# Optimization experiments

Measured on AMD Instinct MI355X. Metric: run time of the kernel, lower is better.

Reference implementation:

```python
import jax, jax.numpy as jnp
import numpy as np

B, T, IN, H = 4096, 19, 17, 1024


def setup_inputs() -> dict:
    key = jax.random.key(0)
    ks = jax.random.split(key, 7)
    s = 0.05
    return {
        "x": jax.random.normal(ks[0], (B, T, IN), dtype=jnp.float32),
        "W_ih": jax.random.normal(ks[1], (4 * H, IN), dtype=jnp.float32) * s,
        "W_hh": jax.random.normal(ks[2], (4 * H, H), dtype=jnp.float32) * s,
        "b_ih": jax.random.normal(ks[3], (4 * H,), dtype=jnp.float32) * s,
        "b_hh": jax.random.normal(ks[4], (4 * H,), dtype=jnp.float32) * s,
        "W_lin": jax.random.normal(ks[5], (IN, H), dtype=jnp.float32) * s,
        "b_lin": jax.random.normal(ks[6], (IN,), dtype=jnp.float32) * s,
    }


def reference(x, W_ih, W_hh, b_ih, b_hh, W_lin, b_lin):
    # x: [B, T, IN]; PyTorch LSTMCell gate order is i, f, g, o.
    batch = x.shape[0]
    hid = W_hh.shape[1]
    h0 = jnp.zeros((batch, hid), dtype=x.dtype)
    c0 = jnp.zeros((batch, hid), dtype=x.dtype)

    def step(carry, xt):
        h, c = carry
        gates = xt @ W_ih.T + b_ih + h @ W_hh.T + b_hh  # [B, 4H]
        i, f, g, o = jnp.split(gates, 4, axis=-1)
        i = jax.nn.sigmoid(i)
        f = jax.nn.sigmoid(f)
        g = jnp.tanh(g)
        o = jax.nn.sigmoid(o)
        c_new = f * c + i * g
        h_new = o * jnp.tanh(c_new)
        out = h_new @ W_lin.T + b_lin  # [B, IN]
        return (h_new, c_new), out

    (h_fin, c_fin), outs = jax.lax.scan(step, (h0, c0), jnp.swapaxes(x, 0, 1))
    output = jnp.swapaxes(outs, 0, 1)  # [B, T, IN]
    return output, h_fin, c_fin
```

## Files before the change

kernel.cpp:

```cpp
#include <hip/hip_runtime.h>
#include <hip/hip_bf16.h>

typedef unsigned short u16;
typedef __attribute__((ext_vector_type(8))) __bf16 bf16x8;
typedef __attribute__((ext_vector_type(8))) short short8;
typedef __attribute__((ext_vector_type(4))) float f32x4;

#define BB 4096
#define TT 19
#define INP 17
#define HH 1024
#define NE 4128
#define NT_PROJ 15

#define ABASE(b) ((b) * 16384)
#define BBASE(b) (32768 + (b) * 16384)
#define PBASE(b) (65536 + (b) * 2048)
#define LDS_BYTES 139264

#define FENCE asm volatile("" ::: "memory")

__device__ __forceinline__ u16 f2bfu(float f) {
    __hip_bfloat16 b = __float2bfloat16(f);
    return __builtin_bit_cast(unsigned short, b);
}
__device__ __forceinline__ float fast_sigmoid(float x) {
    return 1.f / (1.f + __expf(-x));
}
__device__ __forceinline__ float fast_tanh(float x) {
    float e = __expf(2.f * x);
    return (e - 1.f) / (e + 1.f);
}
__device__ __forceinline__ bf16x8 ldfrag(const u16* p) {
    return __builtin_bit_cast(bf16x8, *(const short8*)p);
}
__device__ __forceinline__ void cp16(const u16* l, const void* g) {
    __builtin_amdgcn_global_load_lds(
        (const __attribute__((address_space(1))) unsigned int*)g,
        (__attribute__((address_space(3))) unsigned int*)l, 16, 0, 0);
}

__global__ void prep_wperm(const float* __restrict__ Whh, const float* __restrict__ Wlin,
                           u16* __restrict__ wperm) {
    size_t idx = ((size_t)blockIdx.x * 256 + threadIdx.x) * 8;
    int R = (int)(idx >> 10);
    int k = (int)(idx & 1023);
    const float* src = nullptr;
    if (R < 4096) {
        int nt = R >> 8, r = R & 255;
        int qn = r >> 6, nf = (r >> 4) & 3, cj = r & 15;
        int hcol = nt * 64 + qn * 16 + cj;
        src = Whh + ((size_t)(nf * HH + hcol)) * HH + k;
    } else if (R - 4096 < INP) {
        src = Wlin + (size_t)(R - 4096) * HH + k;
    }
#pragma unroll
    for (int e = 0; e < 8; ++e) wperm[idx + e] = src ? f2bfu(src[e]) : (u16)0;
}

__global__ void prep_wx64(const float* __restrict__ Wih, u16* __restrict__ wx64) {
    int idx = blockIdx.x * 256 + threadIdx.x;
    int R = idx >> 6, k = idx & 63;
    u16 v = 0;
    if (R < 4096 && k < INP) {
        int nt = R >> 8, r = R & 255;
        int qn = r >> 6, nf = (r >> 4) & 3, cj = r & 15;
        int hcol = nt * 64 + qn * 16 + cj;
        v = f2bfu(Wih[(size_t)(nf * HH + hcol) * INP + k]);
    }
    wx64[idx] = v;
}

__global__ void prep_bias(const float* __restrict__ bih, const float* __restrict__ bhh,
                          float* __restrict__ bias) {
    int idx = blockIdx.x * 256 + threadIdx.x;
    bias[idx] = bih[idx] + bhh[idx];
}

__global__ void prep_x64(const float* __restrict__ x, u16* __restrict__ xpad) {
    int idx = blockIdx.x * 256 + threadIdx.x;
    int c = idx & 63;
    int rb = idx >> 6;
    int t = rb >> 12;
    int b = rb & 4095;
    xpad[idx] = (c < INP) ? f2bfu(x[((size_t)b * TT + t) * INP + c]) : (u16)0;
}

__global__ __launch_bounds__(512, 2) void lstm_step(
    const u16* __restrict__ h_in, u16* __restrict__ h_out,
    float* __restrict__ c_buf, const u16* __restrict__ wperm,
    const u16* __restrict__ wx64, const float* __restrict__ bias,
    const u16* __restrict__ xpad64, const float* __restrict__ blin,
    float* __restrict__ outp, float* __restrict__ h_fin,
    int t, int is_last, int tail)
{
    extern __shared__ u16 lds[];

    const int tid = threadIdx.x;
    const int lane = tid & 63;
    const int wv = tid >> 6;
    const int qr = wv >> 2, qn = wv & 3;
    const int r16 = lane & 15, s4 = lane >> 4;

    int mt, nt;
    if (tail) { mt = blockIdx.x; nt = NT_PROJ; }
    else {
        const int xcd = blockIdx.x & 7, local = blockIdx.x >> 3;
        mt = (xcd >> 2) * 8 + (local & 7);
        nt = (xcd & 3) * 4 + (local >> 3);
    }
    const int m0 = mt * 256;
    const size_t R0 = (size_t)nt * 256;
    const bool my_proj = (nt == NT_PROJ) && (qn < 2);

    int srow[4], sgc[4];
#pragma unroll
    for (int i = 0; i < 4; ++i) {
        int d = tid + i * 512;
        srow[i] = d >> 3;
        sgc[i] = (d & 7) ^ (srow[i] & 7);
    }
    const u16* hA[4];
    const u16* wB[4];
#pragma unroll
    for (int i = 0; i < 4; ++i) {
        hA[i] = h_in + (size_t)(m0 + srow[i]) * HH + sgc[i] * 8;
        wB[i] = wperm + (R0 + srow[i]) * HH + sgc[i] * 8;
    }
    const int prow = (tid >> 3) & 31;
    const int pgc = (tid & 7) ^ (prow & 7);
    const u16* wP = wperm + (size_t)(4096 + prow) * HH + pgc * 8;

    int aoff[8], boff[4], poff;
#pragma unroll
    for (int mf = 0; mf < 8; ++mf) {
        int r = qr * 128 + mf * 16 + r16;
        aoff[mf] = r * 64 + ((s4 ^ (r & 7)) * 8);
    }
#pragma unroll
    for (int nf = 0; nf < 4; ++nf) {
        int r = qn * 64 + nf * 16 + r16;
        boff[nf] = r * 64 + ((s4 ^ (r & 7)) * 8);
    }
    {
        int r = qn * 16 + r16;
        poff = r * 64 + ((s4 ^ (r & 7)) * 8);
    }

    f32x4 acc[8][4];
    const int n = nt * 64 + qn * 16 + r16;
    if (!tail) {
#pragma unroll
        for (int nf = 0; nf < 4; ++nf) {
            float bv = bias[nf * HH + n];
#pragma unroll
            for (int mf = 0; mf < 8; ++mf) acc[mf][nf] = (f32x4){bv, bv, bv, bv};
        }
    }
    f32x4 pacc[8];
    const int p = qn * 16 + r16;
    if (my_proj) {
        float pv = (p < INP) ? blin[p] : 0.f;
#pragma unroll
        for (int mf = 0; mf < 8; ++mf) pacc[mf] = (f32x4){pv, pv, pv, pv};
    }

    const u16* xA = xpad64 + ((size_t)t * BB + m0) * 64;
#pragma unroll
    for (int i = 0; i < 4; ++i)
        cp16(&lds[ABASE(0) + (tid + i * 512) * 8], xA + (size_t)srow[i] * 64 + sgc[i] * 8);
#pragma unroll
    for (int i = 0; i < 4; ++i)
        cp16(&lds[BBASE(0) + (tid + i * 512) * 8], wx64 + (R0 + srow[i]) * 64 + sgc[i] * 8);
    if (wv < 4) cp16(&lds[PBASE(0) + tid * 8], wP);

    for (int j = 0; j < 17; ++j) {
        const int cb = j & 1, nb = cb ^ 1;
        if (j < 16) {
            const int ko = j * 64;
#pragma unroll
            for (int i = 0; i < 4; ++i)
                cp16(&lds[ABASE(nb) + (tid + i * 512) * 8], hA[i] + ko);
#pragma unroll
            for (int i = 0; i < 4; ++i)
                cp16(&lds[BBASE(nb) + (tid + i * 512) * 8], wB[i] + ko);
            if (wv < 4) {
                cp16(&lds[PBASE(nb) + tid * 8], wP + ko);
                asm volatile("s_waitcnt vmcnt(9)" ::: "memory");
            } else {
                asm volatile("s_waitcnt vmcnt(8)" ::: "memory");
            }
        } else {
            asm volatile("s_waitcnt vmcnt(0)" ::: "memory");
        }
        __builtin_amdgcn_s_barrier();
        FENCE;

        const int cbA = ABASE(cb), cbB = BBASE(cb), cbP = PBASE(cb);
        const bool do_p = my_proj && (j > 0);
#pragma unroll
        for (int kk = 0; kk < 2; ++kk) {
            const int kx = kk * 32;
            bf16x8 b[4];
            if (!tail) {
#pragma unroll
                for (int nf = 0; nf < 4; ++nf)
                    b[nf] = ldfrag(&lds[cbB + (boff[nf] ^ kx)]);
            }
            bf16x8 pb;
            if (do_p) pb = ldfrag(&lds[cbP + (poff ^ kx)]);
#pragma unroll
            for (int h2 = 0; h2 < 2; ++h2) {
                bf16x8 a[4];
#pragma unroll
                for (int i = 0; i < 4; ++i)
                    a[i] = ldfrag(&lds[cbA + (aoff[h2 * 4 + i] ^ kx)]);
                if (!tail) {
#pragma unroll
                    for (int nf = 0; nf < 4; ++nf)
#pragma unroll
                        for (int i = 0; i < 4; ++i)
                            acc[h2 * 4 + i][nf] = __builtin_amdgcn_mfma_f32_16x16x32_bf16(
                                a[i], b[nf], acc[h2 * 4 + i][nf], 0, 0, 0);
                }
                if (do_p) {
#pragma unroll
                    for (int i = 0; i < 4; ++i)
                        pacc[h2 * 4 + i] = __builtin_amdgcn_mfma_f32_16x16x32_bf16(
                            a[i], pb, pacc[h2 * 4 + i], 0, 0, 0);
                }
            }
        }
        FENCE;
        __builtin_amdgcn_s_barrier();
        FENCE;
    }

    if (!tail) {
#pragma unroll
        for (int mf = 0; mf < 8; ++mf)
#pragma unroll
            for (int j = 0; j < 4; ++j) {
                int row = m0 + qr * 128 + mf * 16 + s4 * 4 + j;
                float iv = fast_sigmoid(acc[mf][0][j]);
                float fv = fast_sigmoid(acc[mf][1][j]);
                float gv = fast_tanh(acc[mf][2][j]);
                float ov = fast_sigmoid(acc[mf][3][j]);
                size_t ci = (size_t)row * HH + n;
                float cold = __builtin_nontemporal_load(&c_buf[ci]);
                float cnew = fv * cold + iv * gv;
                float hnew = ov * fast_tanh(cnew);
                __builtin_nontemporal_store(cnew, &c_buf[ci]);
                h_out[ci] = f2bfu(hnew);
                if (is_last) __builtin_nontemporal_store(hnew, &h_fin[ci]);
            }
    }
    if (my_proj && t > 0 && p < INP) {
#pragma unroll
        for (int mf = 0; mf < 8; ++mf)
#pragma unroll
            for (int j = 0; j < 4; ++j) {
                int row = m0 + qr * 128 + mf * 16 + s4 * 4 + j;
                __builtin_nontemporal_store(
                    pacc[mf][j], &outp[((size_t)row * TT + (t - 1)) * INP + p]);
            }
    }
}

extern "C" void kernel_launch(void* const* d_in, const int* in_sizes, int n_in,
                              void* d_out, int out_size, void* d_ws, size_t ws_size,
                              hipStream_t stream)
{
    const float* x    = (const float*)d_in[0];
    const float* Wih  = (const float*)d_in[1];
    const float* Whh  = (const float*)d_in[2];
    const float* bih  = (const float*)d_in[3];
    const float* bhh  = (const float*)d_in[4];
    const float* Wlin = (const float*)d_in[5];
    const float* blin = (const float*)d_in[6];
    float* out = (float*)d_out;

    char* ws = (char*)d_ws;
    u16* hb0     = (u16*)(ws);
    u16* hb1     = (u16*)(ws +  8388608);
    u16* xpad64  = (u16*)(ws + 16777216);
    u16* wperm   = (u16*)(ws + 27262976);
    u16* wx64    = (u16*)(ws + 35717120);
    float* bias  = (float*)(ws + 36245504);

    float* h_fin = out + (size_t)BB * TT * INP;
    float* c_buf = h_fin + (size_t)BB * HH;

    hipFuncSetAttribute((const void*)lstm_step,
                        hipFuncAttributeMaxDynamicSharedMemorySize, LDS_BYTES);

    hipMemsetAsync(hb0, 0, (size_t)BB * HH * sizeof(u16), stream);
    hipMemsetAsync(c_buf, 0, (size_t)BB * HH * sizeof(float), stream);
    hipMemsetAsync((char*)xpad64 + (size_t)19 * BB * 64 * 2, 0, BB * 64 * 2, stream);

    prep_wperm<<<2064, 256, 0, stream>>>(Whh, Wlin, wperm);
    prep_wx64<<<1032, 256, 0, stream>>>(Wih, wx64);
    prep_bias<<<16, 256, 0, stream>>>(bih, bhh, bias);
    prep_x64<<<19456, 256, 0, stream>>>(x, xpad64);

    for (int t = 0; t < TT; ++t) {
        const u16* hin = (t & 1) ? hb1 : hb0;
        u16* hout = (t & 1) ? hb0 : hb1;
        lstm_step<<<256, 512, LDS_BYTES, stream>>>(
            hin, hout, c_buf, wperm, wx64, bias, xpad64, blin, out,
            h_fin, t, (t == TT - 1) ? 1 : 0, 0);
    }
    lstm_step<<<16, 512, LDS_BYTES, stream>>>(
        hb1, hb0, c_buf, wperm, wx64, bias, xpad64, blin, out,
        h_fin, TT, 0, 1);
}
```

Measured before the change: 1.165 ms.

## Prefetch cell state into LDS and coalesce c/h epilogue stores

```diff
diff --git a/kernel.cpp b/kernel.cpp
--- a/kernel.cpp
+++ b/kernel.cpp
@@ -33,6 +33,9 @@
 }
 __device__ __forceinline__ bf16x8 ldfrag(const u16* p) {
     return __builtin_bit_cast(bf16x8, *(const short8*)p);
+}
+__device__ __forceinline__ int cBase(int row) {
+    return row < 128 ? 16384 + row * 128 : 49152 + (row - 128) * 128;
 }
 __device__ __forceinline__ void cp16(const u16* l, const void* g) {
     __builtin_amdgcn_global_load_lds(
@@ -190,6 +193,15 @@
             } else {
                 asm volatile("s_waitcnt vmcnt(8)" ::: "memory");
             }
+        } else if (!tail) {
+#pragma unroll
+            for (int i = 0; i < 8; ++i) {
+                const int s = tid + i * 512;
+                const int crow = s >> 4, cch = s & 15;
+                const u16* dst = (i < 4) ? &lds[16384 + s * 8] : &lds[32768 + s * 8];
+                cp16(dst, c_buf + (size_t)(m0 + crow) * HH + nt * 64 + cch * 4);
+            }
+            asm volatile("s_waitcnt vmcnt(8)" ::: "memory");
         } else {
             asm volatile("s_waitcnt vmcnt(0)" ::: "memory");
         }
@@ -198,6 +210,7 @@
 
         const int cbA = ABASE(cb), cbB = BBASE(cb), cbP = PBASE(cb);
         const bool do_p = my_proj && (j > 0);
+        __builtin_amdgcn_s_setprio(1);
 #pragma unroll
         for (int kk = 0; kk < 2; ++kk) {
             const int kx = kk * 32;
@@ -231,29 +244,43 @@
                 }
             }
         }
+        __builtin_amdgcn_s_setprio(0);
         FENCE;
         __builtin_amdgcn_s_barrier();
         FENCE;
     }
 
     if (!tail) {
+        asm volatile("s_waitcnt vmcnt(0)" ::: "memory");
+        __syncthreads();
+        const int cl = qn * 16 + r16;
 #pragma unroll
         for (int mf = 0; mf < 8; ++mf)
 #pragma unroll
             for (int j = 0; j < 4; ++j) {
-                int row = m0 + qr * 128 + mf * 16 + s4 * 4 + j;
+                int rl = qr * 128 + mf * 16 + s4 * 4 + j;
                 float iv = fast_sigmoid(acc[mf][0][j]);
                 float fv = fast_sigmoid(acc[mf][1][j]);
                 float gv = fast_tanh(acc[mf][2][j]);
                 float ov = fast_sigmoid(acc[mf][3][j]);
-                size_t ci = (size_t)row * HH + n;
-                float cold = __builtin_nontemporal_load(&c_buf[ci]);
+                float* crow = (float*)&lds[cBase(rl)];
+                float cold = crow[cl];
                 float cnew = fv * cold + iv * gv;
                 float hnew = ov * fast_tanh(cnew);
-                __builtin_nontemporal_store(cnew, &c_buf[ci]);
-                h_out[ci] = f2bfu(hnew);
-                if (is_last) __builtin_nontemporal_store(hnew, &h_fin[ci]);
-            }
+                crow[cl] = cnew;
+                lds[rl * 64 + cl] = f2bfu(hnew);
+                if (is_last)
+                    __builtin_nontemporal_store(
+                        hnew, &h_fin[(size_t)(m0 + rl) * HH + n]);
+            }
+        __syncthreads();
+#pragma unroll 4
+        for (int r = 0; r < 32; ++r) {
+            const int rl = wv * 32 + r;
+            const size_t gi = (size_t)(m0 + rl) * HH + nt * 64 + lane;
+            __builtin_nontemporal_store(((float*)&lds[cBase(rl)])[lane], &c_buf[gi]);
+            h_out[gi] = lds[rl * 64 + lane];
+        }
     }
     if (my_proj && t > 0 && p < INP) {
 #pragma unroll
```

After: 1.027 ms. 11.9% less time.
